# Optimization experiments

Measured on AMD Instinct MI355X. Metric: run time of the kernel, lower is better.

Reference implementation:

```python
import jax, jax.numpy as jnp
import numpy as np

N = 50000
E = 800000
IN_DIM = 256
HID = 128
OUT = 64


def setup_inputs() -> dict:
    key = jax.random.key(0)
    ks = jax.random.split(key, 12)
    inp = {}
    inp["x"] = jax.random.normal(ks[0], (N, IN_DIM), dtype=jnp.float32)
    inp["edge_index"] = jax.random.randint(ks[1], (2, E), 0, N, dtype=jnp.int64)
    s0 = 1.0 / np.sqrt(IN_DIM)
    inp["W0"] = jax.random.uniform(ks[2], (IN_DIM, HID), jnp.float32, -s0, s0)
    inp["b0"] = jax.random.uniform(ks[3], (HID,), jnp.float32, -s0, s0)
    sa = 1.0 / np.sqrt(2 * HID)
    inp["att_w1"] = jax.random.uniform(ks[4], (2 * HID, 1), jnp.float32, -sa, sa)
    inp["att_b1"] = jax.random.uniform(ks[5], (1,), jnp.float32, -sa, sa)
    inp["eps1"] = jnp.float32(0.1)
    inp["att_w2"] = jax.random.uniform(ks[6], (2 * HID, 1), jnp.float32, -sa, sa)
    inp["att_b2"] = jax.random.uniform(ks[7], (1,), jnp.float32, -sa, sa)
    inp["eps2"] = jnp.float32(0.1)
    sc = 1.0 / np.sqrt(HID)
    inp["Wc"] = jax.random.uniform(ks[8], (HID, OUT), jnp.float32, -sc, sc)
    inp["bc"] = jax.random.uniform(ks[9], (OUT,), jnp.float32, -sc, sc)
    return inp


def _fagcn_layer(x, row, col, att_w, att_b, eps):
    # x: [N, H]; row/col: [E]
    x_i = x[row]                       # [E, H] source (gathered)
    x_j = x[col]                       # [E, H] destination
    # cat([x_i, x_j]) @ att_w == x_i @ att_w[:H] + x_j @ att_w[H:]
    H = x.shape[1]
    score = x_i @ att_w[:H] + x_j @ att_w[H:] + att_b  # [E, 1]
    alpha = jnp.tanh(score)            # [E, 1]
    messages = alpha * x_i             # [E, H]
    agg = jax.ops.segment_sum(messages, col, num_segments=x.shape[0])  # [N, H]
    return eps * x + (1.0 - eps) * agg


def reference(x, edge_index, W0, b0, att_w1, att_b1, eps1, att_w2, att_b2, eps2, Wc, bc):
    row, col = edge_index[0], edge_index[1]
    h = jax.nn.relu(x @ W0 + b0)       # initial linear + relu (dropout=eval identity)
    h = jax.nn.relu(_fagcn_layer(h, row, col, att_w1, att_b1, eps1))
    h = jax.nn.relu(_fagcn_layer(h, row, col, att_w2, att_b2, eps2))
    return h @ Wc + bc                 # [N, OUT]
```

## Files before the change

kernel.cpp:

```cpp
#include <hip/hip_runtime.h>

#define N_NODES 50000
#define E_EDGES 800000
#define IN_DIM 256
#define HID 128
#define OUT_DIM 64
#define SLOT 64

#define LR 64
#define KS 64
#define KP 72
#define HP 136

#define NBUILD ((E_EDGES / 8 + 255) / 256)
#define NLIN ((N_NODES + LR - 1) / LR)


typedef unsigned short u16;
typedef __attribute__((ext_vector_type(8))) short short8;
typedef __attribute__((ext_vector_type(4))) float floatx4;

__device__ __forceinline__ u16 f2bf(float f) {
    unsigned u = __float_as_uint(f);
    unsigned r = (u + 0x7FFFu + ((u >> 16) & 1u)) >> 16;
    return (u16)r;
}
__device__ __forceinline__ void bf8_unpack(uint4 v, float* f) {
    f[0] = __uint_as_float(v.x << 16); f[1] = __uint_as_float(v.x & 0xffff0000u);
    f[2] = __uint_as_float(v.y << 16); f[3] = __uint_as_float(v.y & 0xffff0000u);
    f[4] = __uint_as_float(v.z << 16); f[5] = __uint_as_float(v.z & 0xffff0000u);
    f[6] = __uint_as_float(v.w << 16); f[7] = __uint_as_float(v.w & 0xffff0000u);
}
__device__ __forceinline__ uint4 bf8_pack(const float* f) {
    uint4 o;
    o.x = f2bf(f[0]) | ((unsigned)f2bf(f[1]) << 16);
    o.y = f2bf(f[2]) | ((unsigned)f2bf(f[3]) << 16);
    o.z = f2bf(f[4]) | ((unsigned)f2bf(f[5]) << 16);
    o.w = f2bf(f[6]) | ((unsigned)f2bf(f[7]) << 16);
    return o;
}

__global__ __launch_bounds__(256) void k_pre(const float* __restrict__ W0,
                                             const float* __restrict__ Wc,
                                             u16* __restrict__ W0T,
                                             u16* __restrict__ Wct,
                                             int* __restrict__ cnt) {
    const int gid = blockIdx.x * 256 + threadIdx.x;
    if (gid < N_NODES / 4) ((int4*)cnt)[gid] = (int4){0, 0, 0, 0};
    if (gid < IN_DIM * HID) {
        const int n = gid >> 8, k = gid & (IN_DIM - 1);
        W0T[gid] = f2bf(W0[k * HID + n]);
    }
    if (gid < HID * OUT_DIM) {
        const int o = gid >> 7, k = gid & (HID - 1);
        Wct[gid] = f2bf(Wc[k * OUT_DIM + o]);
    }
}

__global__ __launch_bounds__(256) void k_front(
    const float* __restrict__ x, const u16* __restrict__ W0T,
    const float* __restrict__ b0, const float* __restrict__ aw1,
    u16* __restrict__ h, float* __restrict__ sa, float* __restrict__ sb,
    const int* __restrict__ ei, int* __restrict__ cnt,
    u16* __restrict__ srcidx) {
    __shared__ u16 As[LR][KP];
    __shared__ u16 Bs[HID][KP];

    if (blockIdx.x < NBUILD) {
        const int gid = blockIdx.x * 256 + threadIdx.x;
        if (gid >= E_EDGES / 8) return;
        const int4 w0 = ((const int4*)ei)[2 * gid];
        const int4 w1 = ((const int4*)ei)[2 * gid + 1];
        const int4 c0 = ((const int4*)(ei + E_EDGES))[2 * gid];
        const int4 c1 = ((const int4*)(ei + E_EDGES))[2 * gid + 1];
        const int p0 = atomicAdd(&cnt[c0.x], 1);
        const int p1 = atomicAdd(&cnt[c0.y], 1);
        const int p2 = atomicAdd(&cnt[c0.z], 1);
        const int p3 = atomicAdd(&cnt[c0.w], 1);
        const int p4 = atomicAdd(&cnt[c1.x], 1);
        const int p5 = atomicAdd(&cnt[c1.y], 1);
        const int p6 = atomicAdd(&cnt[c1.z], 1);
        const int p7 = atomicAdd(&cnt[c1.w], 1);
        if (p0 < SLOT) srcidx[(c0.x << 6) + p0] = (u16)w0.x;
        if (p1 < SLOT) srcidx[(c0.y << 6) + p1] = (u16)w0.y;
        if (p2 < SLOT) srcidx[(c0.z << 6) + p2] = (u16)w0.z;
        if (p3 < SLOT) srcidx[(c0.w << 6) + p3] = (u16)w0.w;
        if (p4 < SLOT) srcidx[(c1.x << 6) + p4] = (u16)w1.x;
        if (p5 < SLOT) srcidx[(c1.y << 6) + p5] = (u16)w1.y;
        if (p6 < SLOT) srcidx[(c1.z << 6) + p6] = (u16)w1.z;
        if (p7 < SLOT) srcidx[(c1.w << 6) + p7] = (u16)w1.w;
        return;
    }

    const int t = threadIdx.x;
    const int lane = t & 63;
    const int w = t >> 6;
    const int sub = lane & 15;
    const int quad = lane >> 4;
    const int row0 = (blockIdx.x - NBUILD) * LR;

    floatx4 acc[8];
    #pragma unroll
    for (int i = 0; i < 8; ++i) acc[i] = (floatx4){0.f, 0.f, 0.f, 0.f};

    const int ar = t >> 2;
    const int ak = (t & 3) * 16;
    const int sr = t >> 1;
    const int sk = (t & 1) * 32;

    for (int k0 = 0; k0 < IN_DIM; k0 += KS) {
        {
            int gr = row0 + ar;
            if (gr > N_NODES - 1) gr = N_NODES - 1;
            const float* src = x + (size_t)gr * IN_DIM + k0 + ak;
            #pragma unroll
            for (int i = 0; i < 2; ++i) {
                float4 f0 = ((const float4*)src)[2 * i];
                float4 f1 = ((const float4*)src)[2 * i + 1];
                uint4 p;
                p.x = f2bf(f0.x) | ((unsigned)f2bf(f0.y) << 16);
                p.y = f2bf(f0.z) | ((unsigned)f2bf(f0.w) << 16);
                p.z = f2bf(f1.x) | ((unsigned)f2bf(f1.y) << 16);
                p.w = f2bf(f1.z) | ((unsigned)f2bf(f1.w) << 16);
                *(uint4*)&As[ar][ak + 8 * i] = p;
            }
            const u16* wsrc = W0T + (size_t)sr * IN_DIM + k0 + sk;
            #pragma unroll
            for (int i = 0; i < 4; ++i)
                *(uint4*)&Bs[sr][sk + 8 * i] = ((const uint4*)wsrc)[i];
        }
        __syncthreads();
        #pragma unroll
        for (int kk = 0; kk < KS; kk += 32) {
            short8 a0 = *(const short8*)&As[w * 16 + sub][kk + quad * 8];
            #pragma unroll
            for (int ct = 0; ct < 8; ++ct) {
                short8 bb = *(const short8*)&Bs[ct * 16 + sub][kk + quad * 8];
                acc[ct] = __builtin_amdgcn_mfma_f32_16x16x32_bf16(a0, bb, acc[ct], 0, 0, 0);
            }
        }
        __syncthreads();
    }

    float bias[8], w1c[8], w2c[8];
    #pragma unroll
    for (int ct = 0; ct < 8; ++ct) {
        const int col = ct * 16 + sub;
        bias[ct] = b0[col];
        w1c[ct] = aw1[col];
        w2c[ct] = aw1[HID + col];
    }
    #pragma unroll
    for (int reg = 0; reg < 4; ++reg) {
        const int gr = row0 + w * 16 + quad * 4 + reg;
        const bool ok = gr < N_NODES;
        float ps = 0.f, pd = 0.f;
        #pragma unroll
        for (int ct = 0; ct < 8; ++ct) {
            const float val = fmaxf(acc[ct][reg] + bias[ct], 0.f);
            if (ok) h[(size_t)gr * HID + ct * 16 + sub] = f2bf(val);
            ps += val * w1c[ct];
            pd += val * w2c[ct];
        }
        #pragma unroll
        for (int off = 1; off < 16; off <<= 1) {
            ps += __shfl_xor(ps, off);
            pd += __shfl_xor(pd, off);
        }
        if (sub == 0 && ok) { sa[gr] = ps; sb[gr] = pd; }
    }
}

__global__ __launch_bounds__(256) void k_agg(const u16* __restrict__ hin,
                                             const float* __restrict__ sa,
                                             const float* __restrict__ sb,
                                             const float* __restrict__ attb,
                                             const float* __restrict__ epsp,
                                             const int* __restrict__ cnt,
                                             const u16* __restrict__ srcidx,
                                             u16* __restrict__ hout,
                                             const float* __restrict__ attw_next,
                                             float* __restrict__ sa_next,
                                             float* __restrict__ sb_next) {
    const int qid = threadIdx.x >> 4;
    const int sub = threadIdx.x & 15;
    const int n = blockIdx.x * 16 + qid;
    if (n >= N_NODES) return;
    const float b = attb[0];
    const float sbn = sb[n];
    const int beg = n << 6;
    int deg = cnt[n];
    if (deg > SLOT) deg = SLOT;
    const int end = beg + deg;
    float acc[8];
    #pragma unroll
    for (int j = 0; j < 8; ++j) acc[j] = 0.f;

    int e = beg;
    uint4 svn;
    if (e + 8 <= end) svn = *(const uint4*)(srcidx + e);
    for (; e + 8 <= end; e += 8) {
        const uint4 sv = svn;
        if (e + 16 <= end) svn = *(const uint4*)(srcidx + e + 8);
        int s[8];
        s[0] = (int)(sv.x & 0xffffu); s[1] = (int)(sv.x >> 16);
        s[2] = (int)(sv.y & 0xffffu); s[3] = (int)(sv.y >> 16);
        s[4] = (int)(sv.z & 0xffffu); s[5] = (int)(sv.z >> 16);
        s[6] = (int)(sv.w & 0xffffu); s[7] = (int)(sv.w >> 16);
        uint4 v[8];
        #pragma unroll
        for (int i = 0; i < 8; ++i)
            v[i] = *(const uint4*)(hin + (size_t)s[i] * HID + sub * 8);
        const float tt = tanhf(sa[s[sub & 7]] + sbn + b);
        float al[8];
        #pragma unroll
        for (int i = 0; i < 8; ++i) al[i] = __shfl(tt, i, 16);
        #pragma unroll
        for (int i = 0; i < 8; ++i) {
            float f[8];
            bf8_unpack(v[i], f);
            #pragma unroll
            for (int j = 0; j < 8; ++j) acc[j] += al[i] * f[j];
        }
    }
    const int rem = end - e;
    if (rem > 0) {
        const int sfirst = (int)srcidx[e];
        int s[8];
        #pragma unroll
        for (int i = 0; i < 8; ++i) s[i] = (i < rem) ? (int)srcidx[e + i] : sfirst;
        const float tt = ((sub & 7) < rem) ? tanhf(sa[s[sub & 7]] + sbn + b) : 0.f;
        float al[8];
        #pragma unroll
        for (int i = 0; i < 8; ++i) al[i] = __shfl(tt, i, 16);
        #pragma unroll
        for (int i = 0; i < 8; ++i) {
            if (i < rem) {
                const uint4 v = *(const uint4*)(hin + (size_t)s[i] * HID + sub * 8);
                float f[8];
                bf8_unpack(v, f);
                #pragma unroll
                for (int j = 0; j < 8; ++j) acc[j] += al[i] * f[j];
            }
        }
    }

    const float eps = epsp[0];
    const float om = 1.f - eps;
    const uint4 sv = *(const uint4*)(hin + (size_t)n * HID + sub * 8);
    float self[8], hv[8];
    bf8_unpack(sv, self);
    #pragma unroll
    for (int j = 0; j < 8; ++j)
        hv[j] = fmaxf(eps * self[j] + om * acc[j], 0.f);
    *(uint4*)(hout + (size_t)n * HID + sub * 8) = bf8_pack(hv);

    if (attw_next != nullptr) {
        float psum = 0.f, dsum = 0.f;
        #pragma unroll
        for (int j = 0; j < 8; ++j) {
            psum += hv[j] * attw_next[sub * 8 + j];
            dsum += hv[j] * attw_next[HID + sub * 8 + j];
        }
        #pragma unroll
        for (int off = 1; off < 16; off <<= 1) {
            psum += __shfl_xor(psum, off);
            dsum += __shfl_xor(dsum, off);
        }
        if (sub == 0) { sa_next[n] = psum; sb_next[n] = dsum; }
    }
}

__global__ __launch_bounds__(256) void k_out_mfma(const u16* __restrict__ h,
                                                  const u16* __restrict__ Wct,
                                                  const float* __restrict__ bc,
                                                  float* __restrict__ out) {
    __shared__ u16 Hs[LR][HP];
    const int t = threadIdx.x;
    const int lane = t & 63;
    const int w = t >> 6;
    const int sub = lane & 15;
    const int quad = lane >> 4;
    const int row0 = blockIdx.x * LR;

    {
        const int hr = t >> 2;
        const int hc = (t & 3) * 32;
        int gr = row0 + hr;
        if (gr > N_NODES - 1) gr = N_NODES - 1;
        const u16* src = h + (size_t)gr * HID + hc;
        #pragma unroll
        for (int i = 0; i < 4; ++i)
            *(uint4*)&Hs[hr][hc + 8 * i] = ((const uint4*)src)[i];
    }
    __syncthreads();

    floatx4 acc[4];
    #pragma unroll
    for (int j = 0; j < 4; ++j) acc[j] = (floatx4){0.f, 0.f, 0.f, 0.f};

    #pragma unroll
    for (int ks = 0; ks < 4; ++ks) {
        const int ko = ks * 32 + quad * 8;
        short8 a = *(const short8*)&Hs[w * 16 + sub][ko];
        #pragma unroll
        for (int ct = 0; ct < 4; ++ct) {
            short8 bb = *(const short8*)(Wct + (ct * 16 + sub) * HID + ko);
            acc[ct] = __builtin_amdgcn_mfma_f32_16x16x32_bf16(a, bb, acc[ct], 0, 0, 0);
        }
    }

    #pragma unroll
    for (int ct = 0; ct < 4; ++ct) {
        const float bias = bc[ct * 16 + sub];
        #pragma unroll
        for (int reg = 0; reg < 4; ++reg) {
            const int gr = row0 + w * 16 + quad * 4 + reg;
            if (gr < N_NODES)
                out[(size_t)gr * OUT_DIM + ct * 16 + sub] = acc[ct][reg] + bias;
        }
    }
}

extern "C" void kernel_launch(void* const* d_in, const int* in_sizes, int n_in,
                              void* d_out, int out_size, void* d_ws, size_t ws_size,
                              hipStream_t stream) {
    const float* x   = (const float*)d_in[0];
    const int*   ei  = (const int*)d_in[1];
    const float* W0  = (const float*)d_in[2];
    const float* b0  = (const float*)d_in[3];
    const float* aw1 = (const float*)d_in[4];
    const float* ab1 = (const float*)d_in[5];
    const float* e1  = (const float*)d_in[6];
    const float* aw2 = (const float*)d_in[7];
    const float* ab2 = (const float*)d_in[8];
    const float* e2  = (const float*)d_in[9];
    const float* Wc  = (const float*)d_in[10];
    const float* bc  = (const float*)d_in[11];
    float* out = (float*)d_out;

    u16* hA  = (u16*)d_ws;
    u16* hB  = hA + (size_t)N_NODES * HID;
    u16* W0T = hB + (size_t)N_NODES * HID;
    u16* Wct = W0T + IN_DIM * HID;
    float* sa1 = (float*)(Wct + HID * OUT_DIM);
    float* sb1 = sa1 + N_NODES;
    float* sa2 = sb1 + N_NODES;
    float* sb2 = sa2 + N_NODES;
    int* cnt    = (int*)(sb2 + N_NODES);
    u16* srcidx = (u16*)(cnt + N_NODES);

    k_pre<<<128, 256, 0, stream>>>(W0, Wc, W0T, Wct, cnt);
    k_front<<<NBUILD + NLIN, 256, 0, stream>>>(x, W0T, b0, aw1, hA, sa1, sb1,
                                               ei, cnt, srcidx);
    k_agg<<<(N_NODES + 15) / 16, 256, 0, stream>>>(hA, sa1, sb1, ab1, e1, cnt, srcidx,
                                                   hB, aw2, sa2, sb2);
    k_agg<<<(N_NODES + 15) / 16, 256, 0, stream>>>(hB, sa2, sb2, ab2, e2, cnt, srcidx,
                                                   hA, nullptr, nullptr, nullptr);
    k_out_mfma<<<NLIN, 256, 0, stream>>>(hA, Wct, bc, out);
}
```

Measured before the change: 239.3 us.

## Privatize edge bucketing counters per XCD and compact buckets in a separate pass

The CSR-like adjacency build now keeps a separate counter array and a 16-slot sub-bucket per XCD, read from the hardware XCC_ID register. The atomics use workgroup scope, so they avoid cross-XCD coherence traffic on the global counters. A new compact kernel prefix-sums the eight per-XCD counts for each node and merges the sub-buckets into the original 64-slot list plus a degree array. The change adds a kernel launch and a larger counter array to zero. It relies on workgroup-scope atomics being correct when every block on an XCD shares the same L2, and it truncates any node with more than 16 in-edges on one XCD.

```diff
diff --git a/kernel.cpp b/kernel.cpp
--- a/kernel.cpp
+++ b/kernel.cpp
@@ -6,6 +6,7 @@
 #define HID 128
 #define OUT_DIM 64
 #define SLOT 64
+#define RSLOT 16
 
 #define LR 64
 #define KS 64
@@ -44,9 +45,10 @@
                                              const float* __restrict__ Wc,
                                              u16* __restrict__ W0T,
                                              u16* __restrict__ Wct,
-                                             int* __restrict__ cnt) {
+                                             int* __restrict__ cnt8) {
     const int gid = blockIdx.x * 256 + threadIdx.x;
-    if (gid < N_NODES / 4) ((int4*)cnt)[gid] = (int4){0, 0, 0, 0};
+    for (int i = gid; i < 8 * N_NODES / 4; i += 32768)
+        ((int4*)cnt8)[i] = (int4){0, 0, 0, 0};
     if (gid < IN_DIM * HID) {
         const int n = gid >> 8, k = gid & (IN_DIM - 1);
         W0T[gid] = f2bf(W0[k * HID + n]);
@@ -61,34 +63,42 @@
     const float* __restrict__ x, const u16* __restrict__ W0T,
     const float* __restrict__ b0, const float* __restrict__ aw1,
     u16* __restrict__ h, float* __restrict__ sa, float* __restrict__ sb,
-    const int* __restrict__ ei, int* __restrict__ cnt,
-    u16* __restrict__ srcidx) {
+    const int* __restrict__ ei, int* __restrict__ cnt8,
+    u16* __restrict__ srcidx2) {
     __shared__ u16 As[LR][KP];
     __shared__ u16 Bs[HID][KP];
 
     if (blockIdx.x < NBUILD) {
+        int xcd;
+        asm volatile("s_getreg_b32 %0, hwreg(HW_REG_XCC_ID, 0, 32)" : "=s"(xcd));
+        xcd &= 7;
+        const int cbase = xcd * N_NODES;
+        const int rbase = xcd * RSLOT;
         const int gid = blockIdx.x * 256 + threadIdx.x;
         if (gid >= E_EDGES / 8) return;
         const int4 w0 = ((const int4*)ei)[2 * gid];
         const int4 w1 = ((const int4*)ei)[2 * gid + 1];
         const int4 c0 = ((const int4*)(ei + E_EDGES))[2 * gid];
         const int4 c1 = ((const int4*)(ei + E_EDGES))[2 * gid + 1];
-        const int p0 = atomicAdd(&cnt[c0.x], 1);
-        const int p1 = atomicAdd(&cnt[c0.y], 1);
-        const int p2 = atomicAdd(&cnt[c0.z], 1);
-        const int p3 = atomicAdd(&cnt[c0.w], 1);
-        const int p4 = atomicAdd(&cnt[c1.x], 1);
-        const int p5 = atomicAdd(&cnt[c1.y], 1);
-        const int p6 = atomicAdd(&cnt[c1.z], 1);
-        const int p7 = atomicAdd(&cnt[c1.w], 1);
-        if (p0 < SLOT) srcidx[(c0.x << 6) + p0] = (u16)w0.x;
-        if (p1 < SLOT) srcidx[(c0.y << 6) + p1] = (u16)w0.y;
-        if (p2 < SLOT) srcidx[(c0.z << 6) + p2] = (u16)w0.z;
-        if (p3 < SLOT) srcidx[(c0.w << 6) + p3] = (u16)w0.w;
-        if (p4 < SLOT) srcidx[(c1.x << 6) + p4] = (u16)w1.x;
-        if (p5 < SLOT) srcidx[(c1.y << 6) + p5] = (u16)w1.y;
-        if (p6 < SLOT) srcidx[(c1.z << 6) + p6] = (u16)w1.z;
-        if (p7 < SLOT) srcidx[(c1.w << 6) + p7] = (u16)w1.w;
+        #define AADD(c) __hip_atomic_fetch_add(&cnt8[cbase + (c)], 1, \
+                        __ATOMIC_RELAXED, __HIP_MEMORY_SCOPE_WORKGROUP)
+        const int p0 = AADD(c0.x);
+        const int p1 = AADD(c0.y);
+        const int p2 = AADD(c0.z);
+        const int p3 = AADD(c0.w);
+        const int p4 = AADD(c1.x);
+        const int p5 = AADD(c1.y);
+        const int p6 = AADD(c1.z);
+        const int p7 = AADD(c1.w);
+        #undef AADD
+        if (p0 < RSLOT) srcidx2[(c0.x << 7) + rbase + p0] = (u16)w0.x;
+        if (p1 < RSLOT) srcidx2[(c0.y << 7) + rbase + p1] = (u16)w0.y;
+        if (p2 < RSLOT) srcidx2[(c0.z << 7) + rbase + p2] = (u16)w0.z;
+        if (p3 < RSLOT) srcidx2[(c0.w << 7) + rbase + p3] = (u16)w0.w;
+        if (p4 < RSLOT) srcidx2[(c1.x << 7) + rbase + p4] = (u16)w1.x;
+        if (p5 < RSLOT) srcidx2[(c1.y << 7) + rbase + p5] = (u16)w1.y;
+        if (p6 < RSLOT) srcidx2[(c1.z << 7) + rbase + p6] = (u16)w1.z;
+        if (p7 < RSLOT) srcidx2[(c1.w << 7) + rbase + p7] = (u16)w1.w;
         return;
     }
 
@@ -169,6 +179,38 @@
         }
         if (sub == 0 && ok) { sa[gr] = ps; sb[gr] = pd; }
     }
+}
+
+__global__ __launch_bounds__(256) void k_compact(const int* __restrict__ cnt8,
+                                                 const u16* __restrict__ srcidx2,
+                                                 int* __restrict__ deg,
+                                                 u16* __restrict__ srcidx) {
+    const int qid = threadIdx.x >> 4;
+    const int sub = threadIdx.x & 15;
+    const int n = blockIdx.x * 16 + qid;
+    if (n >= N_NODES) return;
+    int c = 0;
+    if (sub < 8) {
+        c = cnt8[sub * N_NODES + n];
+        if (c > RSLOT) c = RSLOT;
+    }
+    int scan = c;
+    #pragma unroll
+    for (int d = 1; d < 8; d <<= 1) {
+        const int tv = __shfl_up(scan, d, 16);
+        if (sub >= d) scan += tv;
+    }
+    const int off = scan - c;
+    const int D = __shfl(scan, 7, 16);
+    if (sub < 8 && c > 0) {
+        const u16* s2 = srcidx2 + ((size_t)n << 7) + (sub << 4);
+        u16* dst = srcidx + ((size_t)n << 6);
+        for (int j = 0; j < c; ++j) {
+            const int dpos = off + j;
+            if (dpos < SLOT) dst[dpos] = s2[j];
+        }
+    }
+    if (sub == 0) deg[n] = D > SLOT ? SLOT : D;
 }
 
 __global__ __launch_bounds__(256) void k_agg(const u16* __restrict__ hin,
@@ -341,21 +383,24 @@
 
     u16* hA  = (u16*)d_ws;
     u16* hB  = hA + (size_t)N_NODES * HID;
+    u16* srcidx2 = hB;
     u16* W0T = hB + (size_t)N_NODES * HID;
     u16* Wct = W0T + IN_DIM * HID;
     float* sa1 = (float*)(Wct + HID * OUT_DIM);
     float* sb1 = sa1 + N_NODES;
     float* sa2 = sb1 + N_NODES;
     float* sb2 = sa2 + N_NODES;
-    int* cnt    = (int*)(sb2 + N_NODES);
-    u16* srcidx = (u16*)(cnt + N_NODES);
-
-    k_pre<<<128, 256, 0, stream>>>(W0, Wc, W0T, Wct, cnt);
+    int* deg    = (int*)(sb2 + N_NODES);
+    u16* srcidx = (u16*)(deg + N_NODES);
+    int* cnt8   = (int*)(srcidx + (size_t)N_NODES * SLOT);
+
+    k_pre<<<128, 256, 0, stream>>>(W0, Wc, W0T, Wct, cnt8);
     k_front<<<NBUILD + NLIN, 256, 0, stream>>>(x, W0T, b0, aw1, hA, sa1, sb1,
-                                               ei, cnt, srcidx);
-    k_agg<<<(N_NODES + 15) / 16, 256, 0, stream>>>(hA, sa1, sb1, ab1, e1, cnt, srcidx,
+                                               ei, cnt8, srcidx2);
+    k_compact<<<(N_NODES + 15) / 16, 256, 0, stream>>>(cnt8, srcidx2, deg, srcidx);
+    k_agg<<<(N_NODES + 15) / 16, 256, 0, stream>>>(hA, sa1, sb1, ab1, e1, deg, srcidx,
                                                    hB, aw2, sa2, sb2);
-    k_agg<<<(N_NODES + 15) / 16, 256, 0, stream>>>(hB, sa2, sb2, ab2, e2, cnt, srcidx,
+    k_agg<<<(N_NODES + 15) / 16, 256, 0, stream>>>(hB, sa2, sb2, ab2, e2, deg, srcidx,
                                                    hA, nullptr, nullptr, nullptr);
     k_out_mfma<<<NLIN, 256, 0, stream>>>(hA, Wct, bc, out);
 }
```

Result: no change. 242.8 us (+1.5%).
